# Kernel optimization log

Measured on AMD Instinct MI355X. Metric: run time of the kernel, lower is better.

The kernel has to match this reference:

```python
import jax, jax.numpy as jnp
import numpy as np

K = 128          # num_clusters (init kwarg k)
N_ITERS = 100    # torch loop runs up to 100 iters; converged centroids are a
                 # fixed point, so running all 100 matches the early-exit result


def _sq_dists(x, c):
    # squared Euclidean distances [N, K]; argmin identical to torch.cdist argmin
    return (jnp.sum(x * x, axis=1, keepdims=True)
            - 2.0 * (x @ c.T)
            + jnp.sum(c * c, axis=1)[None, :])


def _assign_and_update(x, c):
    ids = jnp.argmin(_sq_dists(x, c), axis=1)                     # [N]
    sums = jax.ops.segment_sum(x, ids, num_segments=K)            # [K, D]
    counts = jax.ops.segment_sum(jnp.ones((x.shape[0],), x.dtype), ids,
                                 num_segments=K)                  # [K]
    return ids, sums / counts[:, None]   # mean per cluster (NaN if empty, as in torch)


def setup_inputs() -> dict:
    key = jax.random.key(0)
    kx, kp = jax.random.split(key)
    N, D = 32768, 256
    x = jax.random.normal(kx, (N, D), dtype=jnp.float32)
    # torch.randperm(N)[:K] -> distinct initial centroid indices
    init_idx = jax.random.permutation(kp, N)[:K].astype(jnp.int32)
    return {"x": x, "init_idx": init_idx}


def reference(x, init_idx):
    c0 = x[init_idx]  # [K, D]

    def body(c, _):
        _, newc = _assign_and_update(x, c)
        return newc, None

    # 99 updates, then final assignment + update: returned ids correspond to the
    # centroids BEFORE the last update, exactly like the torch loop's last iter.
    c, _ = jax.lax.scan(body, c0, None, length=N_ITERS - 1)
    ids, c = _assign_and_update(x, c)

    logits = x @ c.T  # temperature = 1.0
    logp = jax.nn.log_softmax(logits, axis=-1)
    # CrossEntropyLoss(mean) with pseudo labels = cluster ids
    loss = -jnp.mean(jnp.take_along_axis(logp, ids[:, None], axis=1))
    return loss
```

## Files before the change

kernel.cpp:

```cpp
#include <hip/hip_runtime.h>
#include <cstdint>

#define NPTS 32768
#define DIM  256
#define NK   128
#define NITER 100
#define NBLK 256
#define NTHR 1024
#define PAD  33

typedef unsigned short ushort_t;
typedef unsigned long long ull_t;
typedef __attribute__((ext_vector_type(8))) short s8v;
typedef __attribute__((ext_vector_type(4))) float f4v;

__device__ __forceinline__ unsigned short f2bf(float f) {
  unsigned u = __float_as_uint(f);
  u += 0x7fffu + ((u >> 16) & 1u);
  return (unsigned short)(u >> 16);
}
__device__ __forceinline__ float bf2f(unsigned short b) {
  return __uint_as_float(((unsigned)b) << 16);
}

__device__ __forceinline__ void cstore(float* p, float v) {
  __hip_atomic_store(p, v, __ATOMIC_RELAXED, __HIP_MEMORY_SCOPE_AGENT);
}
__device__ __forceinline__ float cload(const float* p) {
  return __hip_atomic_load(p, __ATOMIC_RELAXED, __HIP_MEMORY_SCOPE_AGENT);
}
__device__ __forceinline__ void cstorei(int* p, int v) {
  __hip_atomic_store(p, v, __ATOMIC_RELAXED, __HIP_MEMORY_SCOPE_AGENT);
}
__device__ __forceinline__ int cloadi(const int* p) {
  return __hip_atomic_load(p, __ATOMIC_RELAXED, __HIP_MEMORY_SCOPE_AGENT);
}
__device__ __forceinline__ void cstore64(ull_t* p, ull_t v) {
  __hip_atomic_store(p, v, __ATOMIC_RELAXED, __HIP_MEMORY_SCOPE_AGENT);
}
__device__ __forceinline__ ull_t cload64(const ull_t* p) {
  return __hip_atomic_load(p, __ATOMIC_RELAXED, __HIP_MEMORY_SCOPE_AGENT);
}
__device__ __forceinline__ f4v cload128f(const ull_t* p) {
  ull_t a = cload64(p), b = cload64(p + 1);
  f4v r;
  r[0] = __uint_as_float((unsigned)a); r[1] = __uint_as_float((unsigned)(a >> 32));
  r[2] = __uint_as_float((unsigned)b); r[3] = __uint_as_float((unsigned)(b >> 32));
  return r;
}

__device__ __forceinline__ void stage4(const ushort_t* __restrict__ src, s8v* buf, int h, int t) {
  const int lane = t & 63;
  const int wb = (t >> 6) << 6;
#pragma unroll
  for (int i = 0; i < 2; ++i) {
    const int Gb = i * 1024 + wb;
    const int G  = Gb + lane;
    const int Gs = G ^ ((G >> 4) & 7);
    const char* ga = (const char*)src + (G >> 4) * 512 + h * 256 + (Gs & 15) * 16;
    __builtin_amdgcn_global_load_lds(
        (const __attribute__((address_space(1))) void*)ga,
        (__attribute__((address_space(3))) void*)((char*)buf + Gb * 16),
        16, 0, 0);
  }
}

__device__ __forceinline__ void stage_c(const ull_t* __restrict__ cpk,
                                        s8v* bh, s8v* bl, int h, int t) {
#pragma unroll
  for (int i = 0; i < 2; ++i) {
    const int G = i * NTHR + t;
    const int k = G >> 4, gcol = G & 15;
    const int sc2 = gcol ^ (k & 7);
    const ull_t* src = cpk + (size_t)k * 128 + h * 64 + sc2 * 4;
    ull_t w0 = cload64(src + 0), w1 = cload64(src + 1);
    ull_t w2 = cload64(src + 2), w3 = cload64(src + 3);
    s8v vh, vl;
    vh[0] = (short)w0; vl[0] = (short)(w0 >> 16); vh[1] = (short)(w0 >> 32); vl[1] = (short)(w0 >> 48);
    vh[2] = (short)w1; vl[2] = (short)(w1 >> 16); vh[3] = (short)(w1 >> 32); vl[3] = (short)(w1 >> 48);
    vh[4] = (short)w2; vl[4] = (short)(w2 >> 16); vh[5] = (short)(w2 >> 32); vl[5] = (short)(w2 >> 48);
    vh[6] = (short)w3; vl[6] = (short)(w3 >> 16); vh[7] = (short)(w3 >> 32); vl[7] = (short)(w3 >> 48);
    *(s8v*)((char*)bh + G * 16) = vh;
    *(s8v*)((char*)bl + G * 16) = vl;
  }
}

__device__ __forceinline__ void gbar(unsigned* flags, unsigned gen) {
  __syncthreads();
  if (threadIdx.x == 0)
    __hip_atomic_store(&flags[blockIdx.x * 16], gen, __ATOMIC_RELAXED, __HIP_MEMORY_SCOPE_AGENT);
  if (threadIdx.x < NBLK) {
    while (__hip_atomic_load(&flags[threadIdx.x * 16], __ATOMIC_RELAXED, __HIP_MEMORY_SCOPE_AGENT) < gen)
      __builtin_amdgcn_s_sleep(2);
  }
  asm volatile("" ::: "memory");
  __syncthreads();
}
__device__ __forceinline__ void gbar_pf(unsigned* flags, unsigned gen,
    const ushort_t* xhb, const ushort_t* xlb, s8v (*bufs)[2048], int t) {
  __syncthreads();
  stage4(xhb, bufs[0], 0, t);
  stage4(xlb, bufs[1], 0, t);
  if (t == 0)
    __hip_atomic_store(&flags[blockIdx.x * 16], gen, __ATOMIC_RELAXED, __HIP_MEMORY_SCOPE_AGENT);
  if (t < NBLK) {
    while (__hip_atomic_load(&flags[t * 16], __ATOMIC_RELAXED, __HIP_MEMORY_SCOPE_AGENT) < gen)
      __builtin_amdgcn_s_sleep(2);
  }
  asm volatile("" ::: "memory");
  __syncthreads();
}

struct SMa {
  s8v bufs[4][2048];
  float cns[NK];
  float redd[NK * 4];
  int   redk[NK * 4];
  float gmaxs[NK];
  float labvs[NK];
  int   labis[NK];
};
union ScU {
  float accB[NK * PAD];
  float red4[1024];
  float redcn[1024];
};

__device__ __forceinline__ void gemm_core(
    SMa& sm, int t,
    const ushort_t* __restrict__ xhb, const ushort_t* __restrict__ xlb,
    const ull_t* __restrict__ cpk, const float* __restrict__ cn2, f4v (&acc)[2][2]) {
  const int lane = t & 63;
  const int w    = t >> 6;
  const int wr   = w >> 2, wc = w & 3;
  const int g    = lane >> 4, lr = lane & 15;

  if (t < NK) sm.cns[t] = cload(&cn2[2 * t]) + cload(&cn2[2 * t + 1]);

  const f4v zero = {0.f, 0.f, 0.f, 0.f};
#pragma unroll
  for (int i = 0; i < 2; ++i)
#pragma unroll
    for (int j = 0; j < 2; ++j) acc[i][j] = zero;

  const int swz = (lr & 7) << 4;
  int a_off[2], b_off[2];
#pragma unroll
  for (int i = 0; i < 2; ++i) a_off[i] = (wr * 32 + i * 16 + lr) * 256 + g * 16;
#pragma unroll
  for (int j = 0; j < 2; ++j) b_off[j] = (wc * 32 + j * 16 + lr) * 256 + g * 16;

  for (int h = 0; h < 2; ++h) {
    if (h == 1) {
      stage4(xhb, sm.bufs[0], 1, t);
      stage4(xlb, sm.bufs[1], 1, t);
    }
    stage_c(cpk, sm.bufs[2], sm.bufs[3], h, t);
    __syncthreads();
#pragma unroll
    for (int kk = 0; kk < 4; ++kk) {
      s8v ah[2], al[2], bh[2], bl[2];
#pragma unroll
      for (int i = 0; i < 2; ++i) {
        int o = (a_off[i] + kk * 64) ^ swz;
        ah[i] = *(const s8v*)((const char*)sm.bufs[0] + o);
        al[i] = *(const s8v*)((const char*)sm.bufs[1] + o);
      }
#pragma unroll
      for (int j = 0; j < 2; ++j) {
        int o = (b_off[j] + kk * 64) ^ swz;
        bh[j] = *(const s8v*)((const char*)sm.bufs[2] + o);
        bl[j] = *(const s8v*)((const char*)sm.bufs[3] + o);
      }
#pragma unroll
      for (int i = 0; i < 2; ++i)
#pragma unroll
        for (int j = 0; j < 2; ++j) {
          acc[i][j] = __builtin_amdgcn_mfma_f32_16x16x32_bf16(ah[i], bh[j], acc[i][j], 0, 0, 0);
          acc[i][j] = __builtin_amdgcn_mfma_f32_16x16x32_bf16(ah[i], bl[j], acc[i][j], 0, 0, 0);
          acc[i][j] = __builtin_amdgcn_mfma_f32_16x16x32_bf16(al[i], bh[j], acc[i][j], 0, 0, 0);
        }
    }
    if (h == 0) __syncthreads();
  }
}

__global__ __launch_bounds__(NTHR, 1) void kmeans_fused(
    const float* __restrict__ x, const int* __restrict__ init_idx,
    ushort_t* __restrict__ xh, ushort_t* __restrict__ xl,
    ull_t* __restrict__ cpk, float* __restrict__ cn2, int* __restrict__ ids,
    float* __restrict__ psum, float* __restrict__ pcnt,
    float* __restrict__ outp, unsigned* __restrict__ flags,
    float* __restrict__ out) {
  __shared__ SMa sm;
  __shared__ ScU sc;
  __shared__ int idslB[1024];
  __shared__ int cntB[NK];
  __shared__ ushort_t hsm[DIM], lsm[DIM];
  __shared__ float cntsh;

  const int b = blockIdx.x;
  const int t = threadIdx.x;
  const int lane = t & 63;
  const int w  = t >> 6;
  const int wr = w >> 2, wc = w & 3;
  const int g  = lane >> 4, lr = lane & 15;
  const int pbase = b * 128;
  const ushort_t* xhb = xh + (size_t)pbase * DIM;
  const ushort_t* xlb = xl + (size_t)pbase * DIM;
  unsigned gen = 1;

  for (int i = 0; i < 4; ++i) {
    int gg = b * 4096 + i * NTHR + t;
    const float4* src = (const float4*)x + gg * 2;
    float4 fa = src[0], fb = src[1];
    float vv[8] = {fa.x, fa.y, fa.z, fa.w, fb.x, fb.y, fb.z, fb.w};
    s8v vh, vl;
#pragma unroll
    for (int j = 0; j < 8; ++j) {
      unsigned short hh = f2bf(vv[j]);
      vh[j] = (short)hh;
      vl[j] = (short)f2bf(vv[j] - bf2f(hh));
    }
    ((s8v*)xh)[gg] = vh;
    ((s8v*)xl)[gg] = vl;
  }

  if (b < NK) {
    float eff = 0.f;
    if (t < DIM) {
      float v = x[init_idx[b] * DIM + t];
      unsigned short hh = f2bf(v);
      unsigned short ll = f2bf(v - bf2f(hh));
      hsm[t] = hh; lsm[t] = ll;
      eff = bf2f(hh) + bf2f(ll);
    }
    __syncthreads();
    sc.redcn[t] = (t < DIM) ? eff * eff : 0.f;
    if (t < NK) {
      ull_t wv = (ull_t)hsm[2 * t] | ((ull_t)lsm[2 * t] << 16)
               | ((ull_t)hsm[2 * t + 1] << 32) | ((ull_t)lsm[2 * t + 1] << 48);
      cstore64(&cpk[(size_t)b * 128 + t], wv);
    }
    __syncthreads();
    for (int s = 512; s > 0; s >>= 1) { if (t < s) sc.redcn[t] += sc.redcn[t + s]; __syncthreads(); }
    if (t == 0) { cstore(&cn2[b * 2], sc.redcn[0]); cstore(&cn2[b * 2 + 1], 0.f); }
  }
  gbar_pf(flags, gen, xhb, xlb, sm.bufs, t); ++gen;

  for (int it = 0; it < NITER; ++it) {
    {
      f4v acc[2][2];
      gemm_core(sm, t, xhb, xlb, cpk, cn2, acc);
#pragma unroll
      for (int i = 0; i < 2; ++i) {
#pragma unroll
        for (int r = 0; r < 4; ++r) {
          int prow = wr * 32 + i * 16 + g * 4 + r;
          float bd = 1e30f; int bk = 0;
#pragma unroll
          for (int j = 0; j < 2; ++j) {
            int col = wc * 32 + j * 16 + lr;
            float s = sm.cns[col] - 2.f * acc[i][j][r];
            if (s < bd || (s == bd && col < bk)) { bd = s; bk = col; }
          }
#pragma unroll
          for (int msk = 1; msk < 16; msk <<= 1) {
            float od = __shfl_xor(bd, msk, 64);
            int   ok = __shfl_xor(bk, msk, 64);
            if (od < bd || (od == bd && ok < bk)) { bd = od; bk = ok; }
          }
          if (lr == 0) { sm.redd[prow * 4 + wc] = bd; sm.redk[prow * 4 + wc] = bk; }
        }
      }
      __syncthreads();
      if (t < NK) {
        float bd = sm.redd[t * 4]; int bk = sm.redk[t * 4];
#pragma unroll
        for (int q = 1; q < 4; ++q) {
          float dq = sm.redd[t * 4 + q]; int kq = sm.redk[t * 4 + q];
          if (dq < bd || (dq == bd && kq < bk)) { bd = dq; bk = kq; }
        }
        cstorei(&ids[pbase + t], bk);
      }
    }
    gbar(flags, gen); ++gen;

    {
      const int pg = b & 31, dg = b >> 5;
      for (int i = t; i < NK * PAD; i += NTHR) sc.accB[i] = 0.f;
      if (t < NK) cntB[t] = 0;
      idslB[t] = cloadi(&ids[pg * 1024 + t]);
      __syncthreads();
      const int id = idslB[t];
      if (dg == 0) atomicAdd(&cntB[id], 1);
      const ull_t* xr = (const ull_t*)(x + ((size_t)pg * 1024 + t) * DIM + dg * 32);
      f4v v0 = cload128f(xr + 0);
      f4v v1 = cload128f(xr + 2);
      f4v v2 = cload128f(xr + 4);
      f4v v3 = cload128f(xr + 6);
      f4v v4 = cload128f(xr + 8);
      f4v v5 = cload128f(xr + 10);
      f4v v6 = cload128f(xr + 12);
      f4v v7 = cload128f(xr + 14);
      float* ab = &sc.accB[id * PAD];
      atomicAdd(ab + 0,  v0[0]); atomicAdd(ab + 1,  v0[1]); atomicAdd(ab + 2,  v0[2]); atomicAdd(ab + 3,  v0[3]);
      atomicAdd(ab + 4,  v1[0]); atomicAdd(ab + 5,  v1[1]); atomicAdd(ab + 6,  v1[2]); atomicAdd(ab + 7,  v1[3]);
      atomicAdd(ab + 8,  v2[0]); atomicAdd(ab + 9,  v2[1]); atomicAdd(ab + 10, v2[2]); atomicAdd(ab + 11, v2[3]);
      atomicAdd(ab + 12, v3[0]); atomicAdd(ab + 13, v3[1]); atomicAdd(ab + 14, v3[2]); atomicAdd(ab + 15, v3[3]);
      atomicAdd(ab + 16, v4[0]); atomicAdd(ab + 17, v4[1]); atomicAdd(ab + 18, v4[2]); atomicAdd(ab + 19, v4[3]);
      atomicAdd(ab + 20, v5[0]); atomicAdd(ab + 21, v5[1]); atomicAdd(ab + 22, v5[2]); atomicAdd(ab + 23, v5[3]);
      atomicAdd(ab + 24, v6[0]); atomicAdd(ab + 25, v6[1]); atomicAdd(ab + 26, v6[2]); atomicAdd(ab + 27, v6[3]);
      atomicAdd(ab + 28, v7[0]); atomicAdd(ab + 29, v7[1]); atomicAdd(ab + 30, v7[2]); atomicAdd(ab + 31, v7[3]);
      __syncthreads();
#pragma unroll
      for (int s2 = 0; s2 < 4; ++s2) {
        int idx = s2 * NTHR + t;
        int k2 = idx >> 5, dl = idx & 31;
        cstore(&psum[(((size_t)dg * NK + k2) * 32 + pg) * 32 + dl], sc.accB[k2 * PAD + dl]);
      }
      if (dg == 0 && t < NK)
        cstore(&pcnt[(size_t)pg * NK + t], (float)cntB[t]);
    }
    gbar_pf(flags, gen, xhb, xlb, sm.bufs, t); ++gen;

    {
      const int k = b >> 1, hh2 = b & 1;
      const int dwh = t & 127, pch = t >> 7;
      const int dgc = hh2 * 4 + (dwh >> 5), dlc = dwh & 31;
      float s = 0.f;
#pragma unroll
      for (int p2 = pch * 4; p2 < pch * 4 + 4; ++p2)
        s += cload(&psum[(((size_t)dgc * NK + k) * 32 + p2) * 32 + dlc]);
      sc.red4[pch * 128 + dwh] = s;
      float cv = (t < 32) ? cload(&pcnt[(size_t)t * NK + k]) : 0.f;
      if (t < 64) {
#pragma unroll
        for (int m = 1; m < 32; m <<= 1) cv += __shfl_xor(cv, m, 64);
      }
      if (t == 0) cntsh = cv;
      __syncthreads();
      float eff = 0.f;
      if (t < 128) {
        float ssum = 0.f;
#pragma unroll
        for (int ww = 0; ww < 8; ++ww) ssum += sc.red4[ww * 128 + t];
        float mean = ssum / cntsh;
        unsigned short hh = f2bf(mean);
        unsigned short ll = f2bf(mean - bf2f(hh));
        hsm[t] = hh; lsm[t] = ll;
        eff = bf2f(hh) + bf2f(ll);
      }
      __syncthreads();
      sc.redcn[t] = (t < 128) ? eff * eff : 0.f;
      if (t < 64) {
        ull_t wv = (ull_t)hsm[2 * t] | ((ull_t)lsm[2 * t] << 16)
                 | ((ull_t)hsm[2 * t + 1] << 32) | ((ull_t)lsm[2 * t + 1] << 48);
        cstore64(&cpk[(size_t)k * 128 + hh2 * 64 + t], wv);
      }
      __syncthreads();
      for (int st = 512; st > 0; st >>= 1) { if (t < st) sc.redcn[t] += sc.redcn[t + st]; __syncthreads(); }
      if (t == 0) cstore(&cn2[k * 2 + hh2], sc.redcn[0]);
    }
    gbar(flags, gen); ++gen;
  }

  {
    f4v acc[2][2];
    gemm_core(sm, t, xhb, xlb, cpk, cn2, acc);
#pragma unroll
    for (int i = 0; i < 2; ++i) {
#pragma unroll
      for (int r = 0; r < 4; ++r) {
        int prow = wr * 32 + i * 16 + g * 4 + r;
        float m = -1e30f;
#pragma unroll
        for (int j = 0; j < 2; ++j) m = fmaxf(m, acc[i][j][r]);
#pragma unroll
        for (int msk = 1; msk < 16; msk <<= 1) m = fmaxf(m, __shfl_xor(m, msk, 64));
        if (lr == 0) sm.redd[prow * 4 + wc] = m;
      }
    }
    __syncthreads();
    if (t < NK) {
      float m = sm.redd[t * 4];
#pragma unroll
      for (int q = 1; q < 4; ++q) m = fmaxf(m, sm.redd[t * 4 + q]);
      sm.gmaxs[t] = m;
      sm.labis[t] = cloadi(&ids[pbase + t]);
    }
    __syncthreads();
#pragma unroll
    for (int i = 0; i < 2; ++i) {
#pragma unroll
      for (int r = 0; r < 4; ++r) {
        int prow = wr * 32 + i * 16 + g * 4 + r;
        float m = sm.gmaxs[prow];
        int lab = sm.labis[prow];
        float s = 0.f;
#pragma unroll
        for (int j = 0; j < 2; ++j) {
          int col = wc * 32 + j * 16 + lr;
          float v = acc[i][j][r];
          s += expf(v - m);
          if (col == lab) sm.labvs[prow] = v;
        }
#pragma unroll
        for (int msk = 1; msk < 16; msk <<= 1) s += __shfl_xor(s, msk, 64);
        if (lr == 0) sm.redd[prow * 4 + wc] = s;
      }
    }
    __syncthreads();
    if (t < NK) {
      float se = sm.redd[t * 4] + sm.redd[t * 4 + 1] + sm.redd[t * 4 + 2] + sm.redd[t * 4 + 3];
      float lse = sm.gmaxs[t] + logf(se);
      sm.gmaxs[t] = lse - sm.labvs[t];
    }
    __syncthreads();
    if (t == 0) {
      float tot = 0.f;
      for (int q = 0; q < NK; ++q) tot += sm.gmaxs[q];
      cstore(&outp[b], tot);
    }
  }
  gbar(flags, gen); ++gen;
  if (b == 0) {
    sc.redcn[t] = (t < NBLK) ? cload(&outp[t]) : 0.f;
    __syncthreads();
    for (int s = 512; s > 0; s >>= 1) { if (t < s) sc.redcn[t] += sc.redcn[t + s]; __syncthreads(); }
    if (t == 0) out[0] = sc.redcn[0] * (1.0f / (float)NPTS);
  }
}

extern "C" void kernel_launch(void* const* d_in, const int* in_sizes, int n_in,
                              void* d_out, int out_size, void* d_ws, size_t ws_size,
                              hipStream_t stream) {
  const float* x        = (const float*)d_in[0];
  const int*   init_idx = (const int*)d_in[1];
  float* out = (float*)d_out;
  char* ws = (char*)d_ws;

  ushort_t* xh  = (ushort_t*)(ws);
  ushort_t* xl  = (ushort_t*)(ws + 16777216);
  ull_t* cpk  = (ull_t*)(ws + 33554432);
  float* cn2  = (float*)(ws + 33685504);
  int*   ids  = (int*)(ws + 33686528);
  float* psum = (float*)(ws + 33817600);
  float* pcnt = (float*)(ws + 38011904);
  float* outp = (float*)(ws + 38028288);
  unsigned* flags = (unsigned*)(ws + 38029312);

  hipMemsetAsync(flags, 0, 16384, stream);
  kmeans_fused<<<dim3(NBLK), dim3(NTHR), 0, stream>>>(
      x, init_idx, xh, xl, cpk, cn2, ids, psum, pcnt, outp, flags, out);
}
```

Baseline: 7.153 ms.

## Fuse assignment and local partial sums to drop one grid barrier per iteration

Each block now accumulates per-cluster partial sums over its own 128 points right after the argmin, using a swizzled full-width LDS accumulator that aliases the GEMM staging buffers. This removes the global ids write/read and one grid-wide barrier per iteration. In exchange the partial-sum buffer grows to 256 blocks × K × D, and the reduce stage reads 32 MB per iteration instead of 4 MB. Barrier polling is also narrowed to one wavefront with a longer sleep.

```diff
diff --git a/kernel.cpp b/kernel.cpp
--- a/kernel.cpp
+++ b/kernel.cpp
@@ -7,7 +7,6 @@
 #define NITER 100
 #define NBLK 256
 #define NTHR 1024
-#define PAD  33
 
 typedef unsigned short ushort_t;
 typedef unsigned long long ull_t;
@@ -85,14 +84,20 @@
   }
 }
 
+__device__ __forceinline__ void poll_flags(unsigned* flags, unsigned gen, int t) {
+  if (t < 64) {
+#pragma unroll
+    for (int q = 0; q < 4; ++q) {
+      while (__hip_atomic_load(&flags[(q * 64 + t) * 16], __ATOMIC_RELAXED, __HIP_MEMORY_SCOPE_AGENT) < gen)
+        __builtin_amdgcn_s_sleep(8);
+    }
+  }
+}
 __device__ __forceinline__ void gbar(unsigned* flags, unsigned gen) {
   __syncthreads();
   if (threadIdx.x == 0)
     __hip_atomic_store(&flags[blockIdx.x * 16], gen, __ATOMIC_RELAXED, __HIP_MEMORY_SCOPE_AGENT);
-  if (threadIdx.x < NBLK) {
-    while (__hip_atomic_load(&flags[threadIdx.x * 16], __ATOMIC_RELAXED, __HIP_MEMORY_SCOPE_AGENT) < gen)
-      __builtin_amdgcn_s_sleep(2);
-  }
+  poll_flags(flags, gen, threadIdx.x);
   asm volatile("" ::: "memory");
   __syncthreads();
 }
@@ -103,16 +108,16 @@
   stage4(xlb, bufs[1], 0, t);
   if (t == 0)
     __hip_atomic_store(&flags[blockIdx.x * 16], gen, __ATOMIC_RELAXED, __HIP_MEMORY_SCOPE_AGENT);
-  if (t < NBLK) {
-    while (__hip_atomic_load(&flags[t * 16], __ATOMIC_RELAXED, __HIP_MEMORY_SCOPE_AGENT) < gen)
-      __builtin_amdgcn_s_sleep(2);
-  }
+  poll_flags(flags, gen, t);
   asm volatile("" ::: "memory");
   __syncthreads();
 }
 
 struct SMa {
-  s8v bufs[4][2048];
+  union {
+    s8v bufs[4][2048];
+    float accB[NK * DIM];
+  } u;
   float cns[NK];
   float redd[NK * 4];
   int   redk[NK * 4];
@@ -121,7 +126,6 @@
   int   labis[NK];
 };
 union ScU {
-  float accB[NK * PAD];
   float red4[1024];
   float redcn[1024];
 };
@@ -152,10 +156,10 @@
 
   for (int h = 0; h < 2; ++h) {
     if (h == 1) {
-      stage4(xhb, sm.bufs[0], 1, t);
-      stage4(xlb, sm.bufs[1], 1, t);
-    }
-    stage_c(cpk, sm.bufs[2], sm.bufs[3], h, t);
+      stage4(xhb, sm.u.bufs[0], 1, t);
+      stage4(xlb, sm.u.bufs[1], 1, t);
+    }
+    stage_c(cpk, sm.u.bufs[2], sm.u.bufs[3], h, t);
     __syncthreads();
 #pragma unroll
     for (int kk = 0; kk < 4; ++kk) {
@@ -163,14 +167,14 @@
 #pragma unroll
       for (int i = 0; i < 2; ++i) {
         int o = (a_off[i] + kk * 64) ^ swz;
-        ah[i] = *(const s8v*)((const char*)sm.bufs[0] + o);
-        al[i] = *(const s8v*)((const char*)sm.bufs[1] + o);
+        ah[i] = *(const s8v*)((const char*)sm.u.bufs[0] + o);
+        al[i] = *(const s8v*)((const char*)sm.u.bufs[1] + o);
       }
 #pragma unroll
       for (int j = 0; j < 2; ++j) {
         int o = (b_off[j] + kk * 64) ^ swz;
-        bh[j] = *(const s8v*)((const char*)sm.bufs[2] + o);
-        bl[j] = *(const s8v*)((const char*)sm.bufs[3] + o);
+        bh[j] = *(const s8v*)((const char*)sm.u.bufs[2] + o);
+        bl[j] = *(const s8v*)((const char*)sm.u.bufs[3] + o);
       }
 #pragma unroll
       for (int i = 0; i < 2; ++i)
@@ -194,10 +198,10 @@
     float* __restrict__ out) {
   __shared__ SMa sm;
   __shared__ ScU sc;
-  __shared__ int idslB[1024];
+  __shared__ int ids_loc[NK];
   __shared__ int cntB[NK];
+  __shared__ float cnt4[4];
   __shared__ ushort_t hsm[DIM], lsm[DIM];
-  __shared__ float cntsh;
 
   const int b = blockIdx.x;
   const int t = threadIdx.x;
@@ -246,7 +250,7 @@
     for (int s = 512; s > 0; s >>= 1) { if (t < s) sc.redcn[t] += sc.redcn[t + s]; __syncthreads(); }
     if (t == 0) { cstore(&cn2[b * 2], sc.redcn[0]); cstore(&cn2[b * 2 + 1], 0.f); }
   }
-  gbar_pf(flags, gen, xhb, xlb, sm.bufs, t); ++gen;
+  gbar_pf(flags, gen, xhb, xlb, sm.u.bufs, t); ++gen;
 
   for (int it = 0; it < NITER; ++it) {
     {
@@ -281,71 +285,77 @@
           float dq = sm.redd[t * 4 + q]; int kq = sm.redk[t * 4 + q];
           if (dq < bd || (dq == bd && kq < bk)) { bd = dq; bk = kq; }
         }
-        cstorei(&ids[pbase + t], bk);
-      }
-    }
-    gbar(flags, gen); ++gen;
-
-    {
-      const int pg = b & 31, dg = b >> 5;
-      for (int i = t; i < NK * PAD; i += NTHR) sc.accB[i] = 0.f;
+        ids_loc[t] = bk;
+        if (it == NITER - 1) cstorei(&ids[pbase + t], bk);
+      }
+#pragma unroll
+      for (int i = 0; i < 32; ++i) sm.u.accB[i * NTHR + t] = 0.f;
       if (t < NK) cntB[t] = 0;
-      idslB[t] = cloadi(&ids[pg * 1024 + t]);
-      __syncthreads();
-      const int id = idslB[t];
-      if (dg == 0) atomicAdd(&cntB[id], 1);
-      const ull_t* xr = (const ull_t*)(x + ((size_t)pg * 1024 + t) * DIM + dg * 32);
-      f4v v0 = cload128f(xr + 0);
-      f4v v1 = cload128f(xr + 2);
-      f4v v2 = cload128f(xr + 4);
-      f4v v3 = cload128f(xr + 6);
-      f4v v4 = cload128f(xr + 8);
-      f4v v5 = cload128f(xr + 10);
-      f4v v6 = cload128f(xr + 12);
-      f4v v7 = cload128f(xr + 14);
-      float* ab = &sc.accB[id * PAD];
-      atomicAdd(ab + 0,  v0[0]); atomicAdd(ab + 1,  v0[1]); atomicAdd(ab + 2,  v0[2]); atomicAdd(ab + 3,  v0[3]);
-      atomicAdd(ab + 4,  v1[0]); atomicAdd(ab + 5,  v1[1]); atomicAdd(ab + 6,  v1[2]); atomicAdd(ab + 7,  v1[3]);
-      atomicAdd(ab + 8,  v2[0]); atomicAdd(ab + 9,  v2[1]); atomicAdd(ab + 10, v2[2]); atomicAdd(ab + 11, v2[3]);
-      atomicAdd(ab + 12, v3[0]); atomicAdd(ab + 13, v3[1]); atomicAdd(ab + 14, v3[2]); atomicAdd(ab + 15, v3[3]);
-      atomicAdd(ab + 16, v4[0]); atomicAdd(ab + 17, v4[1]); atomicAdd(ab + 18, v4[2]); atomicAdd(ab + 19, v4[3]);
-      atomicAdd(ab + 20, v5[0]); atomicAdd(ab + 21, v5[1]); atomicAdd(ab + 22, v5[2]); atomicAdd(ab + 23, v5[3]);
-      atomicAdd(ab + 24, v6[0]); atomicAdd(ab + 25, v6[1]); atomicAdd(ab + 26, v6[2]); atomicAdd(ab + 27, v6[3]);
-      atomicAdd(ab + 28, v7[0]); atomicAdd(ab + 29, v7[1]); atomicAdd(ab + 30, v7[2]); atomicAdd(ab + 31, v7[3]);
-      __syncthreads();
-#pragma unroll
-      for (int s2 = 0; s2 < 4; ++s2) {
-        int idx = s2 * NTHR + t;
-        int k2 = idx >> 5, dl = idx & 31;
-        cstore(&psum[(((size_t)dg * NK + k2) * 32 + pg) * 32 + dl], sc.accB[k2 * PAD + dl]);
-      }
-      if (dg == 0 && t < NK)
-        cstore(&pcnt[(size_t)pg * NK + t], (float)cntB[t]);
-    }
-    gbar_pf(flags, gen, xhb, xlb, sm.bufs, t); ++gen;
+      __syncthreads();
+      {
+        const int p = t >> 3, dc = t & 7;
+        const int id = ids_loc[p];
+        if (dc == 0) atomicAdd(&cntB[id], 1);
+        const ull_t* xr = (const ull_t*)(x + ((size_t)pbase + p) * DIM + dc * 32);
+        f4v v0 = cload128f(xr + 0),  v1 = cload128f(xr + 2);
+        f4v v2 = cload128f(xr + 4),  v3 = cload128f(xr + 6);
+        f4v v4 = cload128f(xr + 8),  v5 = cload128f(xr + 10);
+        f4v v6 = cload128f(xr + 12), v7 = cload128f(xr + 14);
+        const int sw = (id & 31) ^ ((dc * 4) & 31);
+        float* ab = &sm.u.accB[id * 256 + dc * 32];
+        atomicAdd(&ab[0 ^ sw],  v0[0]); atomicAdd(&ab[1 ^ sw],  v0[1]);
+        atomicAdd(&ab[2 ^ sw],  v0[2]); atomicAdd(&ab[3 ^ sw],  v0[3]);
+        atomicAdd(&ab[4 ^ sw],  v1[0]); atomicAdd(&ab[5 ^ sw],  v1[1]);
+        atomicAdd(&ab[6 ^ sw],  v1[2]); atomicAdd(&ab[7 ^ sw],  v1[3]);
+        atomicAdd(&ab[8 ^ sw],  v2[0]); atomicAdd(&ab[9 ^ sw],  v2[1]);
+        atomicAdd(&ab[10 ^ sw], v2[2]); atomicAdd(&ab[11 ^ sw], v2[3]);
+        atomicAdd(&ab[12 ^ sw], v3[0]); atomicAdd(&ab[13 ^ sw], v3[1]);
+        atomicAdd(&ab[14 ^ sw], v3[2]); atomicAdd(&ab[15 ^ sw], v3[3]);
+        atomicAdd(&ab[16 ^ sw], v4[0]); atomicAdd(&ab[17 ^ sw], v4[1]);
+        atomicAdd(&ab[18 ^ sw], v4[2]); atomicAdd(&ab[19 ^ sw], v4[3]);
+        atomicAdd(&ab[20 ^ sw], v5[0]); atomicAdd(&ab[21 ^ sw], v5[1]);
+        atomicAdd(&ab[22 ^ sw], v5[2]); atomicAdd(&ab[23 ^ sw], v5[3]);
+        atomicAdd(&ab[24 ^ sw], v6[0]); atomicAdd(&ab[25 ^ sw], v6[1]);
+        atomicAdd(&ab[26 ^ sw], v6[2]); atomicAdd(&ab[27 ^ sw], v6[3]);
+        atomicAdd(&ab[28 ^ sw], v7[0]); atomicAdd(&ab[29 ^ sw], v7[1]);
+        atomicAdd(&ab[30 ^ sw], v7[2]); atomicAdd(&ab[31 ^ sw], v7[3]);
+      }
+      __syncthreads();
+#pragma unroll
+      for (int i = 0; i < 32; ++i) {
+        int idx = i * NTHR + t;
+        int k2 = idx >> 8, d2 = idx & 255;
+        int dc2 = d2 >> 5, j2 = d2 & 31;
+        float v = sm.u.accB[k2 * 256 + dc2 * 32 + (j2 ^ (k2 & 31) ^ ((dc2 * 4) & 31))];
+        cstore(&psum[(size_t)b * (NK * DIM) + idx], v);
+      }
+      if (t < NK) cstore(&pcnt[(size_t)b * NK + t], (float)cntB[t]);
+    }
+    gbar_pf(flags, gen, xhb, xlb, sm.u.bufs, t); ++gen;
 
     {
       const int k = b >> 1, hh2 = b & 1;
-      const int dwh = t & 127, pch = t >> 7;
-      const int dgc = hh2 * 4 + (dwh >> 5), dlc = dwh & 31;
+      const int pbq = t >> 7, dwh = t & 127;
+      const int d = hh2 * 128 + dwh;
       float s = 0.f;
-#pragma unroll
-      for (int p2 = pch * 4; p2 < pch * 4 + 4; ++p2)
-        s += cload(&psum[(((size_t)dgc * NK + k) * 32 + p2) * 32 + dlc]);
-      sc.red4[pch * 128 + dwh] = s;
-      float cv = (t < 32) ? cload(&pcnt[(size_t)t * NK + k]) : 0.f;
-      if (t < 64) {
-#pragma unroll
-        for (int m = 1; m < 32; m <<= 1) cv += __shfl_xor(cv, m, 64);
-      }
-      if (t == 0) cntsh = cv;
+#pragma unroll 8
+      for (int pb = pbq * 32; pb < pbq * 32 + 32; ++pb)
+        s += cload(&psum[(size_t)pb * (NK * DIM) + k * 256 + d]);
+      sc.red4[pbq * 128 + dwh] = s;
+      float cv = (t < NBLK) ? cload(&pcnt[(size_t)t * NK + k]) : 0.f;
+      if (t < NBLK) {
+#pragma unroll
+        for (int m = 1; m < 64; m <<= 1) cv += __shfl_xor(cv, m, 64);
+        if (lane == 0) cnt4[w] = cv;
+      }
       __syncthreads();
       float eff = 0.f;
       if (t < 128) {
+        float cnt = cnt4[0] + cnt4[1] + cnt4[2] + cnt4[3];
         float ssum = 0.f;
 #pragma unroll
         for (int ww = 0; ww < 8; ++ww) ssum += sc.red4[ww * 128 + t];
-        float mean = ssum / cntsh;
+        float mean = ssum / cnt;
         unsigned short hh = f2bf(mean);
         unsigned short ll = f2bf(mean - bf2f(hh));
         hsm[t] = hh; lsm[t] = ll;
@@ -446,9 +456,9 @@
   float* cn2  = (float*)(ws + 33685504);
   int*   ids  = (int*)(ws + 33686528);
   float* psum = (float*)(ws + 33817600);
-  float* pcnt = (float*)(ws + 38011904);
-  float* outp = (float*)(ws + 38028288);
-  unsigned* flags = (unsigned*)(ws + 38029312);
+  float* pcnt = (float*)(ws + 67372032);
+  float* outp = (float*)(ws + 67503104);
+  unsigned* flags = (unsigned*)(ws + 67504128);
 
   hipMemsetAsync(flags, 0, 16384, stream);
   kmeans_fused<<<dim3(NBLK), dim3(NTHR), 0, stream>>>(
```

Result: slower. 9.756 ms (+36.4%).

## Keep split-bf16 point tiles resident in LDS and stream centroids in chunks

Applied to the files above, without the earlier changes.

Each block now converts its 128 points to hi/lo bf16 once and keeps them resident in a swizzled LDS buffer for all iterations. This removes the global xh/xl workspace and the per-iteration re-staging of point tiles. Centroids are loaded in eight small K-chunks with plain loads into a padded LDS tile, which adds a syncthreads per chunk. The grid barrier now polls with one wavefront and a longer sleep, and issues a threadfence only after centroid updates so plain (non-atomic) centroid loads see fresh data; this relies on the fence for correctness.

```diff
diff --git a/kernel.cpp b/kernel.cpp
--- a/kernel.cpp
+++ b/kernel.cpp
@@ -38,104 +38,48 @@
 __device__ __forceinline__ void cstore64(ull_t* p, ull_t v) {
   __hip_atomic_store(p, v, __ATOMIC_RELAXED, __HIP_MEMORY_SCOPE_AGENT);
 }
-__device__ __forceinline__ ull_t cload64(const ull_t* p) {
-  return __hip_atomic_load(p, __ATOMIC_RELAXED, __HIP_MEMORY_SCOPE_AGENT);
-}
 __device__ __forceinline__ f4v cload128f(const ull_t* p) {
-  ull_t a = cload64(p), b = cload64(p + 1);
+  ull_t a = __hip_atomic_load(p, __ATOMIC_RELAXED, __HIP_MEMORY_SCOPE_AGENT);
+  ull_t b = __hip_atomic_load(p + 1, __ATOMIC_RELAXED, __HIP_MEMORY_SCOPE_AGENT);
   f4v r;
   r[0] = __uint_as_float((unsigned)a); r[1] = __uint_as_float((unsigned)(a >> 32));
   r[2] = __uint_as_float((unsigned)b); r[3] = __uint_as_float((unsigned)(b >> 32));
   return r;
 }
 
-__device__ __forceinline__ void stage4(const ushort_t* __restrict__ src, s8v* buf, int h, int t) {
-  const int lane = t & 63;
-  const int wb = (t >> 6) << 6;
-#pragma unroll
-  for (int i = 0; i < 2; ++i) {
-    const int Gb = i * 1024 + wb;
-    const int G  = Gb + lane;
-    const int Gs = G ^ ((G >> 4) & 7);
-    const char* ga = (const char*)src + (G >> 4) * 512 + h * 256 + (Gs & 15) * 16;
-    __builtin_amdgcn_global_load_lds(
-        (const __attribute__((address_space(1))) void*)ga,
-        (__attribute__((address_space(3))) void*)((char*)buf + Gb * 16),
-        16, 0, 0);
-  }
-}
-
-__device__ __forceinline__ void stage_c(const ull_t* __restrict__ cpk,
-                                        s8v* bh, s8v* bl, int h, int t) {
-#pragma unroll
-  for (int i = 0; i < 2; ++i) {
-    const int G = i * NTHR + t;
-    const int k = G >> 4, gcol = G & 15;
-    const int sc2 = gcol ^ (k & 7);
-    const ull_t* src = cpk + (size_t)k * 128 + h * 64 + sc2 * 4;
-    ull_t w0 = cload64(src + 0), w1 = cload64(src + 1);
-    ull_t w2 = cload64(src + 2), w3 = cload64(src + 3);
-    s8v vh, vl;
-    vh[0] = (short)w0; vl[0] = (short)(w0 >> 16); vh[1] = (short)(w0 >> 32); vl[1] = (short)(w0 >> 48);
-    vh[2] = (short)w1; vl[2] = (short)(w1 >> 16); vh[3] = (short)(w1 >> 32); vl[3] = (short)(w1 >> 48);
-    vh[4] = (short)w2; vl[4] = (short)(w2 >> 16); vh[5] = (short)(w2 >> 32); vl[5] = (short)(w2 >> 48);
-    vh[6] = (short)w3; vl[6] = (short)(w3 >> 16); vh[7] = (short)(w3 >> 32); vl[7] = (short)(w3 >> 48);
-    *(s8v*)((char*)bh + G * 16) = vh;
-    *(s8v*)((char*)bl + G * 16) = vl;
-  }
-}
-
-__device__ __forceinline__ void gbar(unsigned* flags, unsigned gen) {
+__device__ __forceinline__ void gbar(unsigned* flags, unsigned gen, bool inv) {
   __syncthreads();
   if (threadIdx.x == 0)
     __hip_atomic_store(&flags[blockIdx.x * 16], gen, __ATOMIC_RELAXED, __HIP_MEMORY_SCOPE_AGENT);
-  if (threadIdx.x < NBLK) {
-    while (__hip_atomic_load(&flags[threadIdx.x * 16], __ATOMIC_RELAXED, __HIP_MEMORY_SCOPE_AGENT) < gen)
-      __builtin_amdgcn_s_sleep(2);
-  }
+  if (threadIdx.x < 64) {
+#pragma unroll
+    for (int q = 0; q < 4; ++q) {
+      while (__hip_atomic_load(&flags[(q * 64 + threadIdx.x) * 16], __ATOMIC_RELAXED, __HIP_MEMORY_SCOPE_AGENT) < gen)
+        __builtin_amdgcn_s_sleep(8);
+    }
+  }
+  __syncthreads();
+  if (inv && threadIdx.x == 0) __threadfence();
   asm volatile("" ::: "memory");
   __syncthreads();
 }
-__device__ __forceinline__ void gbar_pf(unsigned* flags, unsigned gen,
-    const ushort_t* xhb, const ushort_t* xlb, s8v (*bufs)[2048], int t) {
-  __syncthreads();
-  stage4(xhb, bufs[0], 0, t);
-  stage4(xlb, bufs[1], 0, t);
-  if (t == 0)
-    __hip_atomic_store(&flags[blockIdx.x * 16], gen, __ATOMIC_RELAXED, __HIP_MEMORY_SCOPE_AGENT);
-  if (t < NBLK) {
-    while (__hip_atomic_load(&flags[t * 16], __ATOMIC_RELAXED, __HIP_MEMORY_SCOPE_AGENT) < gen)
-      __builtin_amdgcn_s_sleep(2);
-  }
-  asm volatile("" ::: "memory");
-  __syncthreads();
-}
-
-struct SMa {
-  s8v bufs[4][2048];
-  float cns[NK];
-  float redd[NK * 4];
-  int   redk[NK * 4];
-  float gmaxs[NK];
-  float labvs[NK];
-  int   labis[NK];
+
+union StU {
+  struct { char ch[128 * 80]; char cl[128 * 80]; } a;
+  struct { float accB[NK * PAD]; ushort_t idsl16[1024]; } b;
+  struct { float red4[1024]; float redcn[1024]; } c;
 };
-union ScU {
-  float accB[NK * PAD];
-  float red4[1024];
-  float redcn[1024];
-};
 
 __device__ __forceinline__ void gemm_core(
-    SMa& sm, int t,
-    const ushort_t* __restrict__ xhb, const ushort_t* __restrict__ xlb,
+    const s8v* __restrict__ xhR, const s8v* __restrict__ xlR,
+    StU& u, float* cns, int t,
     const ull_t* __restrict__ cpk, const float* __restrict__ cn2, f4v (&acc)[2][2]) {
   const int lane = t & 63;
   const int w    = t >> 6;
   const int wr   = w >> 2, wc = w & 3;
   const int g    = lane >> 4, lr = lane & 15;
 
-  if (t < NK) sm.cns[t] = cload(&cn2[2 * t]) + cload(&cn2[2 * t + 1]);
+  if (t < NK) cns[t] = cload(&cn2[2 * t]) + cload(&cn2[2 * t + 1]);
 
   const f4v zero = {0.f, 0.f, 0.f, 0.f};
 #pragma unroll
@@ -143,59 +87,63 @@
 #pragma unroll
     for (int j = 0; j < 2; ++j) acc[i][j] = zero;
 
-  const int swz = (lr & 7) << 4;
-  int a_off[2], b_off[2];
-#pragma unroll
-  for (int i = 0; i < 2; ++i) a_off[i] = (wr * 32 + i * 16 + lr) * 256 + g * 16;
-#pragma unroll
-  for (int j = 0; j < 2; ++j) b_off[j] = (wc * 32 + j * 16 + lr) * 256 + g * 16;
-
-  for (int h = 0; h < 2; ++h) {
-    if (h == 1) {
-      stage4(xhb, sm.bufs[0], 1, t);
-      stage4(xlb, sm.bufs[1], 1, t);
-    }
-    stage_c(cpk, sm.bufs[2], sm.bufs[3], h, t);
-    __syncthreads();
-#pragma unroll
-    for (int kk = 0; kk < 4; ++kk) {
-      s8v ah[2], al[2], bh[2], bl[2];
-#pragma unroll
-      for (int i = 0; i < 2; ++i) {
-        int o = (a_off[i] + kk * 64) ^ swz;
-        ah[i] = *(const s8v*)((const char*)sm.bufs[0] + o);
-        al[i] = *(const s8v*)((const char*)sm.bufs[1] + o);
-      }
+  for (int q = 0; q < 8; ++q) {
+    if (t < 512) {
+      int row = t >> 2, c = t & 3;
+      const ull_t* src = cpk + (size_t)row * 128 + q * 16 + c * 4;
+      ull_t w0 = src[0], w1 = src[1], w2 = src[2], w3 = src[3];
+      s8v vh, vl;
+      vh[0] = (short)w0; vl[0] = (short)(w0 >> 16); vh[1] = (short)(w0 >> 32); vl[1] = (short)(w0 >> 48);
+      vh[2] = (short)w1; vl[2] = (short)(w1 >> 16); vh[3] = (short)(w1 >> 32); vl[3] = (short)(w1 >> 48);
+      vh[4] = (short)w2; vl[4] = (short)(w2 >> 16); vh[5] = (short)(w2 >> 32); vl[5] = (short)(w2 >> 48);
+      vh[6] = (short)w3; vl[6] = (short)(w3 >> 16); vh[7] = (short)(w3 >> 32); vl[7] = (short)(w3 >> 48);
+      *(s8v*)(u.a.ch + row * 80 + c * 16) = vh;
+      *(s8v*)(u.a.cl + row * 80 + c * 16) = vl;
+    }
+    __syncthreads();
+    s8v ah[2], al[2], bh[2], bl[2];
+#pragma unroll
+    for (int i = 0; i < 2; ++i) {
+      int ra = wr * 32 + i * 16 + lr;
+      int o = ra * 512 + (((q * 4 + g) ^ (lr & 7)) * 16);
+      ah[i] = *(const s8v*)((const char*)xhR + o);
+      al[i] = *(const s8v*)((const char*)xlR + o);
+    }
+#pragma unroll
+    for (int j = 0; j < 2; ++j) {
+      int rb = wc * 32 + j * 16 + lr;
+      int o = rb * 80 + g * 16;
+      bh[j] = *(const s8v*)(u.a.ch + o);
+      bl[j] = *(const s8v*)(u.a.cl + o);
+    }
+#pragma unroll
+    for (int i = 0; i < 2; ++i)
 #pragma unroll
       for (int j = 0; j < 2; ++j) {
-        int o = (b_off[j] + kk * 64) ^ swz;
-        bh[j] = *(const s8v*)((const char*)sm.bufs[2] + o);
-        bl[j] = *(const s8v*)((const char*)sm.bufs[3] + o);
-      }
-#pragma unroll
-      for (int i = 0; i < 2; ++i)
-#pragma unroll
-        for (int j = 0; j < 2; ++j) {
-          acc[i][j] = __builtin_amdgcn_mfma_f32_16x16x32_bf16(ah[i], bh[j], acc[i][j], 0, 0, 0);
-          acc[i][j] = __builtin_amdgcn_mfma_f32_16x16x32_bf16(ah[i], bl[j], acc[i][j], 0, 0, 0);
-          acc[i][j] = __builtin_amdgcn_mfma_f32_16x16x32_bf16(al[i], bh[j], acc[i][j], 0, 0, 0);
-        }
-    }
-    if (h == 0) __syncthreads();
+        acc[i][j] = __builtin_amdgcn_mfma_f32_16x16x32_bf16(ah[i], bh[j], acc[i][j], 0, 0, 0);
+        acc[i][j] = __builtin_amdgcn_mfma_f32_16x16x32_bf16(ah[i], bl[j], acc[i][j], 0, 0, 0);
+        acc[i][j] = __builtin_amdgcn_mfma_f32_16x16x32_bf16(al[i], bh[j], acc[i][j], 0, 0, 0);
+      }
+    __syncthreads();
   }
 }
 
 __global__ __launch_bounds__(NTHR, 1) void kmeans_fused(
     const float* __restrict__ x, const int* __restrict__ init_idx,
-    ushort_t* __restrict__ xh, ushort_t* __restrict__ xl,
     ull_t* __restrict__ cpk, float* __restrict__ cn2, int* __restrict__ ids,
     float* __restrict__ psum, float* __restrict__ pcnt,
     float* __restrict__ outp, unsigned* __restrict__ flags,
     float* __restrict__ out) {
-  __shared__ SMa sm;
-  __shared__ ScU sc;
-  __shared__ int idslB[1024];
-  __shared__ int cntB[NK];
+  __shared__ s8v xhR[4096];
+  __shared__ s8v xlR[4096];
+  __shared__ StU u;
+  __shared__ float cns[NK];
+  __shared__ float redd[NK * 4];
+  __shared__ int   redk[NK * 4];
+  __shared__ float gmaxs[NK];
+  __shared__ float labvs[NK];
+  __shared__ int   labis[NK];
+  __shared__ int   cntB[NK];
   __shared__ ushort_t hsm[DIM], lsm[DIM];
   __shared__ float cntsh;
 
@@ -206,13 +154,12 @@
   const int wr = w >> 2, wc = w & 3;
   const int g  = lane >> 4, lr = lane & 15;
   const int pbase = b * 128;
-  const ushort_t* xhb = xh + (size_t)pbase * DIM;
-  const ushort_t* xlb = xl + (size_t)pbase * DIM;
   unsigned gen = 1;
 
   for (int i = 0; i < 4; ++i) {
-    int gg = b * 4096 + i * NTHR + t;
-    const float4* src = (const float4*)x + gg * 2;
+    int G = i * NTHR + t;
+    int row = G >> 5, c = G & 31;
+    const float4* src = (const float4*)(x + ((size_t)pbase + row) * DIM + c * 8);
     float4 fa = src[0], fb = src[1];
     float vv[8] = {fa.x, fa.y, fa.z, fa.w, fb.x, fb.y, fb.z, fb.w};
     s8v vh, vl;
@@ -222,8 +169,9 @@
       vh[j] = (short)hh;
       vl[j] = (short)f2bf(vv[j] - bf2f(hh));
     }
-    ((s8v*)xh)[gg] = vh;
-    ((s8v*)xl)[gg] = vl;
+    int pos = c ^ (row & 7);
+    *(s8v*)((char*)xhR + row * 512 + pos * 16) = vh;
+    *(s8v*)((char*)xlR + row * 512 + pos * 16) = vl;
   }
 
   if (b < NK) {
@@ -236,22 +184,22 @@
       eff = bf2f(hh) + bf2f(ll);
     }
     __syncthreads();
-    sc.redcn[t] = (t < DIM) ? eff * eff : 0.f;
+    u.c.redcn[t] = (t < DIM) ? eff * eff : 0.f;
     if (t < NK) {
       ull_t wv = (ull_t)hsm[2 * t] | ((ull_t)lsm[2 * t] << 16)
                | ((ull_t)hsm[2 * t + 1] << 32) | ((ull_t)lsm[2 * t + 1] << 48);
       cstore64(&cpk[(size_t)b * 128 + t], wv);
     }
     __syncthreads();
-    for (int s = 512; s > 0; s >>= 1) { if (t < s) sc.redcn[t] += sc.redcn[t + s]; __syncthreads(); }
-    if (t == 0) { cstore(&cn2[b * 2], sc.redcn[0]); cstore(&cn2[b * 2 + 1], 0.f); }
-  }
-  gbar_pf(flags, gen, xhb, xlb, sm.bufs, t); ++gen;
+    for (int s = 512; s > 0; s >>= 1) { if (t < s) u.c.redcn[t] += u.c.redcn[t + s]; __syncthreads(); }
+    if (t == 0) { cstore(&cn2[b * 2], u.c.redcn[0]); cstore(&cn2[b * 2 + 1], 0.f); }
+  }
+  gbar(flags, gen, true); ++gen;
 
   for (int it = 0; it < NITER; ++it) {
     {
       f4v acc[2][2];
-      gemm_core(sm, t, xhb, xlb, cpk, cn2, acc);
+      gemm_core(xhR, xlR, u, cns, t, cpk, cn2, acc);
 #pragma unroll
       for (int i = 0; i < 2; ++i) {
 #pragma unroll
@@ -261,7 +209,7 @@
 #pragma unroll
           for (int j = 0; j < 2; ++j) {
             int col = wc * 32 + j * 16 + lr;
-            float s = sm.cns[col] - 2.f * acc[i][j][r];
+            float s = cns[col] - 2.f * acc[i][j][r];
             if (s < bd || (s == bd && col < bk)) { bd = s; bk = col; }
           }
 #pragma unroll
@@ -270,40 +218,36 @@
             int   ok = __shfl_xor(bk, msk, 64);
             if (od < bd || (od == bd && ok < bk)) { bd = od; bk = ok; }
           }
-          if (lr == 0) { sm.redd[prow * 4 + wc] = bd; sm.redk[prow * 4 + wc] = bk; }
+          if (lr == 0) { redd[prow * 4 + wc] = bd; redk[prow * 4 + wc] = bk; }
         }
       }
       __syncthreads();
       if (t < NK) {
-        float bd = sm.redd[t * 4]; int bk = sm.redk[t * 4];
+        float bd = redd[t * 4]; int bk = redk[t * 4];
 #pragma unroll
         for (int q = 1; q < 4; ++q) {
-          float dq = sm.redd[t * 4 + q]; int kq = sm.redk[t * 4 + q];
+          float dq = redd[t * 4 + q]; int kq = redk[t * 4 + q];
           if (dq < bd || (dq == bd && kq < bk)) { bd = dq; bk = kq; }
         }
         cstorei(&ids[pbase + t], bk);
       }
     }
-    gbar(flags, gen); ++gen;
+    gbar(flags, gen, false); ++gen;
 
     {
       const int pg = b & 31, dg = b >> 5;
-      for (int i = t; i < NK * PAD; i += NTHR) sc.accB[i] = 0.f;
+      for (int i = t; i < NK * PAD; i += NTHR) u.b.accB[i] = 0.f;
       if (t < NK) cntB[t] = 0;
-      idslB[t] = cloadi(&ids[pg * 1024 + t]);
-      __syncthreads();
-      const int id = idslB[t];
+      u.b.idsl16[t] = (ushort_t)cloadi(&ids[pg * 1024 + t]);
+      __syncthreads();
+      const int id = u.b.idsl16[t];
       if (dg == 0) atomicAdd(&cntB[id], 1);
       const ull_t* xr = (const ull_t*)(x + ((size_t)pg * 1024 + t) * DIM + dg * 32);
-      f4v v0 = cload128f(xr + 0);
-      f4v v1 = cload128f(xr + 2);
-      f4v v2 = cload128f(xr + 4);
-      f4v v3 = cload128f(xr + 6);
-      f4v v4 = cload128f(xr + 8);
-      f4v v5 = cload128f(xr + 10);
-      f4v v6 = cload128f(xr + 12);
-      f4v v7 = cload128f(xr + 14);
-      float* ab = &sc.accB[id * PAD];
+      f4v v0 = cload128f(xr + 0),  v1 = cload128f(xr + 2);
+      f4v v2 = cload128f(xr + 4),  v3 = cload128f(xr + 6);
+      f4v v4 = cload128f(xr + 8),  v5 = cload128f(xr + 10);
+      f4v v6 = cload128f(xr + 12), v7 = cload128f(xr + 14);
+      float* ab = &u.b.accB[id * PAD];
       atomicAdd(ab + 0,  v0[0]); atomicAdd(ab + 1,  v0[1]); atomicAdd(ab + 2,  v0[2]); atomicAdd(ab + 3,  v0[3]);
       atomicAdd(ab + 4,  v1[0]); atomicAdd(ab + 5,  v1[1]); atomicAdd(ab + 6,  v1[2]); atomicAdd(ab + 7,  v1[3]);
       atomicAdd(ab + 8,  v2[0]); atomicAdd(ab + 9,  v2[1]); atomicAdd(ab + 10, v2[2]); atomicAdd(ab + 11, v2[3]);
@@ -317,12 +261,12 @@
       for (int s2 = 0; s2 < 4; ++s2) {
         int idx = s2 * NTHR + t;
         int k2 = idx >> 5, dl = idx & 31;
-        cstore(&psum[(((size_t)dg * NK + k2) * 32 + pg) * 32 + dl], sc.accB[k2 * PAD + dl]);
+        cstore(&psum[(((size_t)dg * NK + k2) * 32 + pg) * 32 + dl], u.b.accB[k2 * PAD + dl]);
       }
       if (dg == 0 && t < NK)
         cstore(&pcnt[(size_t)pg * NK + t], (float)cntB[t]);
     }
-    gbar_pf(flags, gen, xhb, xlb, sm.bufs, t); ++gen;
+    gbar(flags, gen, false); ++gen;
 
     {
       const int k = b >> 1, hh2 = b & 1;
@@ -332,7 +276,7 @@
 #pragma unroll
       for (int p2 = pch * 4; p2 < pch * 4 + 4; ++p2)
         s += cload(&psum[(((size_t)dgc * NK + k) * 32 + p2) * 32 + dlc]);
-      sc.red4[pch * 128 + dwh] = s;
+      u.c.red4[pch * 128 + dwh] = s;
       float cv = (t < 32) ? cload(&pcnt[(size_t)t * NK + k]) : 0.f;
       if (t < 64) {
 #pragma unroll
@@ -344,7 +288,7 @@
       if (t < 128) {
         float ssum = 0.f;
 #pragma unroll
-        for (int ww = 0; ww < 8; ++ww) ssum += sc.red4[ww * 128 + t];
+        for (int ww = 0; ww < 8; ++ww) ssum += u.c.red4[ww * 128 + t];
         float mean = ssum / cntsh;
         unsigned short hh = f2bf(mean);
         unsigned short ll = f2bf(mean - bf2f(hh));
@@ -352,22 +296,22 @@
         eff = bf2f(hh) + bf2f(ll);
       }
       __syncthreads();
-      sc.redcn[t] = (t < 128) ? eff * eff : 0.f;
+      u.c.redcn[t] = (t < 128) ? eff * eff : 0.f;
       if (t < 64) {
         ull_t wv = (ull_t)hsm[2 * t] | ((ull_t)lsm[2 * t] << 16)
                  | ((ull_t)hsm[2 * t + 1] << 32) | ((ull_t)lsm[2 * t + 1] << 48);
         cstore64(&cpk[(size_t)k * 128 + hh2 * 64 + t], wv);
       }
       __syncthreads();
-      for (int st = 512; st > 0; st >>= 1) { if (t < st) sc.redcn[t] += sc.redcn[t + st]; __syncthreads(); }
-      if (t == 0) cstore(&cn2[k * 2 + hh2], sc.redcn[0]);
-    }
-    gbar(flags, gen); ++gen;
+      for (int st = 512; st > 0; st >>= 1) { if (t < st) u.c.redcn[t] += u.c.redcn[t + st]; __syncthreads(); }
+      if (t == 0) cstore(&cn2[k * 2 + hh2], u.c.redcn[0]);
+    }
+    gbar(flags, gen, true); ++gen;
   }
 
   {
     f4v acc[2][2];
-    gemm_core(sm, t, xhb, xlb, cpk, cn2, acc);
+    gemm_core(xhR, xlR, u, cns, t, cpk, cn2, acc);
 #pragma unroll
     for (int i = 0; i < 2; ++i) {
 #pragma unroll
@@ -378,16 +322,16 @@
         for (int j = 0; j < 2; ++j) m = fmaxf(m, acc[i][j][r]);
 #pragma unroll
         for (int msk = 1; msk < 16; msk <<= 1) m = fmaxf(m, __shfl_xor(m, msk, 64));
-        if (lr == 0) sm.redd[prow * 4 + wc] = m;
+        if (lr == 0) redd[prow * 4 + wc] = m;
       }
     }
     __syncthreads();
     if (t < NK) {
-      float m = sm.redd[t * 4];
-#pragma unroll
-      for (int q = 1; q < 4; ++q) m = fmaxf(m, sm.redd[t * 4 + q]);
-      sm.gmaxs[t] = m;
-      sm.labis[t] = cloadi(&ids[pbase + t]);
+      float m = redd[t * 4];
+#pragma unroll
+      for (int q = 1; q < 4; ++q) m = fmaxf(m, redd[t * 4 + q]);
+      gmaxs[t] = m;
+      labis[t] = cloadi(&ids[pbase + t]);
     }
     __syncthreads();
 #pragma unroll
@@ -395,40 +339,40 @@
 #pragma unroll
       for (int r = 0; r < 4; ++r) {
         int prow = wr * 32 + i * 16 + g * 4 + r;
-        float m = sm.gmaxs[prow];
-        int lab = sm.labis[prow];
+        float m = gmaxs[prow];
+        int lab = labis[prow];
         float s = 0.f;
 #pragma unroll
         for (int j = 0; j < 2; ++j) {
           int col = wc * 32 + j * 16 + lr;
           float v = acc[i][j][r];
           s += expf(v - m);
-          if (col == lab) sm.labvs[prow] = v;
+          if (col == lab) labvs[prow] = v;
         }
 #pragma unroll
         for (int msk = 1; msk < 16; msk <<= 1) s += __shfl_xor(s, msk, 64);
-        if (lr == 0) sm.redd[prow * 4 + wc] = s;
+        if (lr == 0) redd[prow * 4 + wc] = s;
       }
     }
     __syncthreads();
     if (t < NK) {
-      float se = sm.redd[t * 4] + sm.redd[t * 4 + 1] + sm.redd[t * 4 + 2] + sm.redd[t * 4 + 3];
-      float lse = sm.gmaxs[t] + logf(se);
-      sm.gmaxs[t] = lse - sm.labvs[t];
+      float se = redd[t * 4] + redd[t * 4 + 1] + redd[t * 4 + 2] + redd[t * 4 + 3];
+      float lse = gmaxs[t] + logf(se);
+      gmaxs[t] = lse - labvs[t];
     }
     __syncthreads();
     if (t == 0) {
       float tot = 0.f;
-      for (int q = 0; q < NK; ++q) tot += sm.gmaxs[q];
+      for (int q = 0; q < NK; ++q) tot += gmaxs[q];
       cstore(&outp[b], tot);
     }
   }
-  gbar(flags, gen); ++gen;
+  gbar(flags, gen, false); ++gen;
   if (b == 0) {
-    sc.redcn[t] = (t < NBLK) ? cload(&outp[t]) : 0.f;
-    __syncthreads();
-    for (int s = 512; s > 0; s >>= 1) { if (t < s) sc.redcn[t] += sc.redcn[t + s]; __syncthreads(); }
-    if (t == 0) out[0] = sc.redcn[0] * (1.0f / (float)NPTS);
+    u.c.redcn[t] = (t < NBLK) ? cload(&outp[t]) : 0.f;
+    __syncthreads();
+    for (int s = 512; s > 0; s >>= 1) { if (t < s) u.c.redcn[t] += u.c.redcn[t + s]; __syncthreads(); }
+    if (t == 0) out[0] = u.c.redcn[0] * (1.0f / (float)NPTS);
   }
 }
 
@@ -440,17 +384,15 @@
   float* out = (float*)d_out;
   char* ws = (char*)d_ws;
 
-  ushort_t* xh  = (ushort_t*)(ws);
-  ushort_t* xl  = (ushort_t*)(ws + 16777216);
-  ull_t* cpk  = (ull_t*)(ws + 33554432);
-  float* cn2  = (float*)(ws + 33685504);
-  int*   ids  = (int*)(ws + 33686528);
-  float* psum = (float*)(ws + 33817600);
-  float* pcnt = (float*)(ws + 38011904);
-  float* outp = (float*)(ws + 38028288);
-  unsigned* flags = (unsigned*)(ws + 38029312);
+  ull_t* cpk  = (ull_t*)(ws);
+  float* cn2  = (float*)(ws + 131072);
+  int*   ids  = (int*)(ws + 132096);
+  float* psum = (float*)(ws + 263168);
+  float* pcnt = (float*)(ws + 4457472);
+  float* outp = (float*)(ws + 4473856);
+  unsigned* flags = (unsigned*)(ws + 4474880);
 
   hipMemsetAsync(flags, 0, 16384, stream);
   kmeans_fused<<<dim3(NBLK), dim3(NTHR), 0, stream>>>(
-      x, init_idx, xh, xl, cpk, cn2, ids, psum, pcnt, outp, flags, out);
-}
+      x, init_idx, cpk, cn2, ids, psum, pcnt, outp, flags, out);
+}
```

Result: slower. 7.534 ms (+5.3%).
